# Kernel tuning notes

Measured on AMD Instinct MI355X. Metric: run time of the kernel, lower is better.

Reference implementation:

```python
import jax, jax.numpy as jnp
import numpy as np

B, T, D, H, O = 32768, 96, 7, 3, 7

def setup_inputs() -> dict:
    key = jax.random.key(0)
    ks = jax.random.split(key, 7)
    s_ih = 1.0 / np.sqrt(H)
    inp = {
        "x": jax.random.normal(ks[0], (B, T, D), dtype=jnp.float32),
        # PyTorch nn.LSTM params (gate order i,f,g,o), uniform(-1/sqrt(H), 1/sqrt(H))
        "W_ih": jax.random.uniform(ks[1], (4 * H, D), jnp.float32, -s_ih, s_ih),
        "W_hh": jax.random.uniform(ks[2], (4 * H, H), jnp.float32, -s_ih, s_ih),
        "b_ih": jax.random.uniform(ks[3], (4 * H,), jnp.float32, -s_ih, s_ih),
        "b_hh": jax.random.uniform(ks[4], (4 * H,), jnp.float32, -s_ih, s_ih),
        # nn.Linear(H*T, O*T): weight [out,in]
        "W_lin": jax.random.uniform(ks[5], (O * T, H * T), jnp.float32, -1.0 / np.sqrt(H * T), 1.0 / np.sqrt(H * T)),
        "b_lin": jax.random.uniform(ks[6], (O * T,), jnp.float32, -1.0 / np.sqrt(H * T), 1.0 / np.sqrt(H * T)),
    }
    return inp

def _lstm(x, W_ih, W_hh, b_ih, b_hh):
    b = x.shape[0]
    h0 = jnp.zeros((b, H), x.dtype)
    c0 = jnp.zeros((b, H), x.dtype)
    bias = b_ih + b_hh

    def step(carry, x_t):
        h, c = carry
        gates = x_t @ W_ih.T + h @ W_hh.T + bias  # [b, 4H]
        i, f, g, o = jnp.split(gates, 4, axis=-1)
        i = jax.nn.sigmoid(i)
        f = jax.nn.sigmoid(f)
        g = jnp.tanh(g)
        o = jax.nn.sigmoid(o)
        c = f * c + i * g
        h = o * jnp.tanh(c)
        return (h, c), h

    (_, _), hs = jax.lax.scan(step, (h0, c0), jnp.swapaxes(x, 0, 1))  # hs: [T, b, H]
    return jnp.swapaxes(hs, 0, 1)  # [b, T, H]

def reference(x, W_ih, W_hh, b_ih, b_hh, W_lin, b_lin):
    out = _lstm(x, W_ih, W_hh, b_ih, b_hh)            # [B, T, H]
    out = out.reshape(x.shape[0], -1)                  # [B, T*H]
    out = out @ W_lin.T + b_lin                        # [B, O*T]
    return out.reshape(x.shape)                        # [B, T, D]
```

## Files before the change

kernel.cpp:

```cpp
#include <hip/hip_runtime.h>
#include <stdint.h>

typedef unsigned short u16;
typedef unsigned int u32;
typedef __attribute__((ext_vector_type(8))) __bf16 bf16x8;
typedef __attribute__((ext_vector_type(4))) float f32x4;

#define B_TOT   32768
#define T_SEQ   96
#define D_IN    7
#define K_LIN   288
#define N_LIN   672
#define N_PAD   768

#define LOG2E      1.4426950408889634f
#define TWO_LOG2E  2.8853900817779268f

__device__ __forceinline__ u16 f2bf(float f) {
  u32 u = __builtin_bit_cast(u32, f);
  u += 0x7fffu + ((u >> 16) & 1u);
  return (u16)(u >> 16);
}
template<int Q>
__device__ __forceinline__ float qbcast(float v) {
  int i = __builtin_bit_cast(int, v);
  i = __builtin_amdgcn_update_dpp(0, i, Q * 0x55, 0xF, 0xF, true);
  return __builtin_bit_cast(float, i);
}
template<int CTRL>
__device__ __forceinline__ float rdpp(float v) {
  int i = __builtin_bit_cast(int, v);
  i = __builtin_amdgcn_update_dpp(0, i, CTRL, 0xF, 0xF, true);
  return __builtin_bit_cast(float, i);
}

__global__ __launch_bounds__(256) void convert_kernel(
    const float* __restrict__ Wlin, const float* __restrict__ blin,
    u16* __restrict__ Bw, float* __restrict__ biasp)
{
  int i = blockIdx.x * 256 + threadIdx.x;
  if (i < N_PAD * K_LIN) {
    int n = i / K_LIN;
    int kk = i - n * K_LIN;
    int jm = kk / T_SEQ;
    int tm = kk - jm * T_SEQ;
    Bw[i] = f2bf((n < N_LIN) ? Wlin[n * K_LIN + tm * 3 + jm] : 0.0f);
  }
  if (i < N_PAD) biasp[i] = (i < N_LIN) ? blin[i] : 0.0f;
}

__device__ __forceinline__ void steps8_gp(
    const float* __restrict__ xc,
    float& h, float& c,
    const float (&wih)[7], const float (&whr)[4], float bias,
    float sel_s, float sel_b, float* hv8)
{
#pragma unroll
  for (int s = 0; s < 8; ++s) {
    float z = bias;
#pragma unroll
    for (int k = 0; k < 7; ++k) z = fmaf(xc[s * 7 + k], wih[k], z);
    float r1 = rdpp<0x124>(h);
    float r2 = rdpp<0x128>(h);
    float r3 = rdpp<0x12C>(h);
    z = fmaf(h,  whr[0], z);
    z = fmaf(r1, whr[1], z);
    z = fmaf(r2, whr[2], z);
    z = fmaf(r3, whr[3], z);
    float sg = __builtin_amdgcn_rcpf(1.0f + __builtin_amdgcn_exp2f(z));
    float a = fmaf(sel_s, sg, sel_b);
    float ai = qbcast<0>(a);
    float af = qbcast<1>(a);
    float ag = qbcast<2>(a);
    float ao = qbcast<3>(a);
    c = fmaf(af, c, ai * ag);
    float t = 1.0f - 2.0f * __builtin_amdgcn_rcpf(1.0f + __builtin_amdgcn_exp2f(c * TWO_LOG2E));
    float hv = ao * t;
    hv8[s] = hv;
    h = hv;
  }
}

__global__ __launch_bounds__(256, 8) void lstm_kernel(
    const float* __restrict__ x,
    const float* __restrict__ Wih, const float* __restrict__ Whh,
    const float* __restrict__ bih, const float* __restrict__ bhh,
    u16* __restrict__ hs)
{
  __shared__ float sW[132];
  __shared__ __align__(16) float xb[2][16 * 56];

  const int tid = threadIdx.x;
  for (int i = tid; i < 132; i += 256) {
    float v; int row;
    if (i < 84)       { v = Wih[i];       row = i / 7; }
    else if (i < 120) { v = Whh[i - 84];  row = (i - 84) / 3; }
    else              { v = bih[i - 120] + bhh[i - 120]; row = i - 120; }
    const int G = row / 3;
    sW[i] = v * ((G == 2) ? -TWO_LOG2E : -LOG2E);
  }
  __syncthreads();

  const int sub = tid & 15;
  const int g   = sub & 3;
  const int q   = sub >> 2;
  const int jj  = (q < 3) ? q : 2;
  const int row = g * 3 + jj;

  float wih[7];
#pragma unroll
  for (int k = 0; k < 7; ++k) wih[k] = sW[row * 7 + k];
  float bias = sW[120 + row];

  float pv = (float)q;
  float pr = rdpp<0x124>(pv);
  const int delta = (((int)pr) - q) & 3;

  float whr[4];
  whr[0] = (q < 3) ? sW[84 + row * 3 + q] : 0.0f;
#pragma unroll
  for (int r = 1; r < 4; ++r) {
    const int su = (q + r * delta) & 3;
    whr[r] = (su < 3) ? sW[84 + row * 3 + su] : 0.0f;
  }
  const float sel_s = (g == 2) ? 2.0f : 1.0f;
  const float sel_b = (g == 2) ? -1.0f : 0.0f;
#pragma unroll
  for (int k = 0; k < 7; ++k) asm volatile("" : "+v"(wih[k]));
#pragma unroll
  for (int r = 0; r < 4; ++r) asm volatile("" : "+v"(whr[r]));
  asm volatile("" : "+v"(bias));

  const int b0 = blockIdx.x * 16;
  const bool stager = (tid < 224);
  const int sch = tid / 14;
  const int sof = (tid % 14) * 4;
  const float* gbase = x + (size_t)(b0 + sch) * (T_SEQ * D_IN) + sof;
  float* xw0 = &xb[0][tid * 4];
  float* xw1 = &xb[1][tid * 4];

  const int cc = tid >> 4;
  const float* xc0 = &xb[0][cc * 56];
  const float* xc1 = &xb[1][cc * 56];

  u16* __restrict__ hrow = hs + (size_t)(b0 + cc) * K_LIN + jj * T_SEQ;
  const bool writer = (g == 0) && (q < 3);

  float h = 0.f, c = 0.f;
  float hv8[8];

  if (stager) *(float4*)xw0 = *(const float4*)gbase;
  __syncthreads();

#pragma unroll 1
  for (int n2 = 0; n2 < 6; ++n2) {
    const int n = n2 * 2;
    {
      float4 gpre = {};
      if (stager) gpre = *(const float4*)(gbase + (n + 1) * 56);
      steps8_gp(xc0, h, c, wih, whr, bias, sel_s, sel_b, hv8);
      __builtin_amdgcn_sched_barrier(0);
      if (stager) *(float4*)xw1 = gpre;
      if (writer) {
        u32 w0_, w1_, w2_, w3_;
        asm("v_cvt_pk_bf16_f32 %0, %1, %2" : "=v"(w0_) : "v"(hv8[0]), "v"(hv8[1]));
        asm("v_cvt_pk_bf16_f32 %0, %1, %2" : "=v"(w1_) : "v"(hv8[2]), "v"(hv8[3]));
        asm("v_cvt_pk_bf16_f32 %0, %1, %2" : "=v"(w2_) : "v"(hv8[4]), "v"(hv8[5]));
        asm("v_cvt_pk_bf16_f32 %0, %1, %2" : "=v"(w3_) : "v"(hv8[6]), "v"(hv8[7]));
        uint4 pkv; pkv.x = w0_; pkv.y = w1_; pkv.z = w2_; pkv.w = w3_;
        *(uint4*)(hrow + n * 8) = pkv;
      }
      __syncthreads();
    }
    {
      const bool hn = (n2 < 5);
      float4 gpre = {};
      if (stager && hn) gpre = *(const float4*)(gbase + (n + 2) * 56);
      steps8_gp(xc1, h, c, wih, whr, bias, sel_s, sel_b, hv8);
      __builtin_amdgcn_sched_barrier(0);
      if (stager && hn) *(float4*)xw0 = gpre;
      if (writer) {
        u32 w0_, w1_, w2_, w3_;
        asm("v_cvt_pk_bf16_f32 %0, %1, %2" : "=v"(w0_) : "v"(hv8[0]), "v"(hv8[1]));
        asm("v_cvt_pk_bf16_f32 %0, %1, %2" : "=v"(w1_) : "v"(hv8[2]), "v"(hv8[3]));
        asm("v_cvt_pk_bf16_f32 %0, %1, %2" : "=v"(w2_) : "v"(hv8[4]), "v"(hv8[5]));
        asm("v_cvt_pk_bf16_f32 %0, %1, %2" : "=v"(w3_) : "v"(hv8[6]), "v"(hv8[7]));
        uint4 pkv; pkv.x = w0_; pkv.y = w1_; pkv.z = w2_; pkv.w = w3_;
        *(uint4*)(hrow + (n + 1) * 8) = pkv;
      }
      __syncthreads();
    }
  }
}

__device__ __forceinline__ void gload16(const u16* g, u16* l) {
  __builtin_amdgcn_global_load_lds(
      (const __attribute__((address_space(1))) void*)g,
      (__attribute__((address_space(3))) void*)l, 16, 0, 0);
}

__global__ __launch_bounds__(256) void gemm_kernel(
    const u16* __restrict__ A, const u16* __restrict__ Bw,
    const float* __restrict__ bias, float* __restrict__ C)
{
  __shared__ u16 As[128 * 32];
  __shared__ u16 Bs[128 * 32];
  const int tid  = threadIdx.x;
  const int lane = tid & 63;
  const int wid  = tid >> 6;
  const int wm = wid >> 1, wn = wid & 1;

  int bx = blockIdx.x;
  int swzb = (bx & 7) * 192 + (bx >> 3);
  const int bm = swzb / 6;
  const int bn = swzb - bm * 6;
  const size_t m0 = (size_t)bm * 128;
  const int n0 = bn * 128;

  const int ra = tid >> 2;
  const int ca = (tid & 3) * 8;
  const u16* ga = A  + (m0 + (size_t)ra) * K_LIN + ca;
  const u16* gb = Bw + (size_t)(n0 + ra) * K_LIN + ca;
  u16* lA = &As[wid * 512];
  u16* lB = &Bs[wid * 512];

  const int l15 = lane & 15, l4 = lane >> 4;
  const u16* pAf = &As[(wm * 64 + l15) * 32 + l4 * 8];
  const u16* pBf = &Bs[(wn * 64 + l15) * 32 + l4 * 8];

  f32x4 acc[4][4] = {};

  for (int kt = 0; kt < 9; ++kt) {
    const int ko = kt * 32;
    gload16(ga + ko,               lA);
    gload16(ga + 64 * K_LIN + ko,  lA + 2048);
    gload16(gb + ko,               lB);
    gload16(gb + 64 * K_LIN + ko,  lB + 2048);
    __syncthreads();
    bf16x8 af[4], bfv[4];
#pragma unroll
    for (int i = 0; i < 4; ++i) af[i]  = *(const bf16x8*)(const void*)(pAf + i * 512);
#pragma unroll
    for (int i = 0; i < 4; ++i) bfv[i] = *(const bf16x8*)(const void*)(pBf + i * 512);
#pragma unroll
    for (int mi = 0; mi < 4; ++mi)
#pragma unroll
      for (int ni = 0; ni < 4; ++ni)
        acc[mi][ni] = __builtin_amdgcn_mfma_f32_16x16x32_bf16(af[mi], bfv[ni], acc[mi][ni], 0, 0, 0);
    __syncthreads();
  }

  float bv[4];
#pragma unroll
  for (int ni = 0; ni < 4; ++ni) bv[ni] = bias[n0 + wn * 64 + ni * 16 + l15];

#pragma unroll
  for (int mi = 0; mi < 4; ++mi) {
#pragma unroll
    for (int ni = 0; ni < 4; ++ni) {
      const int col = n0 + wn * 64 + ni * 16 + l15;
      if (col < N_LIN) {
#pragma unroll
        for (int r = 0; r < 4; ++r) {
          const size_t row = m0 + wm * 64 + mi * 16 + l4 * 4 + r;
          C[row * N_LIN + col] = acc[mi][ni][r] + bv[ni];
        }
      }
    }
  }
}

extern "C" void kernel_launch(void* const* d_in, const int* in_sizes, int n_in,
                              void* d_out, int out_size, void* d_ws, size_t ws_size,
                              hipStream_t stream) {
  const float* x    = (const float*)d_in[0];
  const float* Wih  = (const float*)d_in[1];
  const float* Whh  = (const float*)d_in[2];
  const float* bih  = (const float*)d_in[3];
  const float* bhh  = (const float*)d_in[4];
  const float* Wlin = (const float*)d_in[5];
  const float* blin = (const float*)d_in[6];
  float* out = (float*)d_out;

  u16* hs = (u16*)d_ws;
  u16* Bw = (u16*)((char*)d_ws + (size_t)B_TOT * K_LIN * 2);
  float* biasp = (float*)((char*)d_ws + (size_t)B_TOT * K_LIN * 2 + (size_t)N_PAD * K_LIN * 2);

  convert_kernel<<<(N_PAD * K_LIN + 255) / 256, 256, 0, stream>>>(Wlin, blin, Bw, biasp);
  lstm_kernel<<<B_TOT / 16, 256, 0, stream>>>(x, Wih, Whh, bih, bhh, hs);
  gemm_kernel<<<(B_TOT / 128) * (N_PAD / 128), 256, 0, stream>>>(hs, Bw, biasp, out);
}
```

Measured before the change: 82.39 us.

## Process two batch rows per lane with packed f32x2 math in LSTM

```diff
diff --git a/kernel.cpp b/kernel.cpp
--- a/kernel.cpp
+++ b/kernel.cpp
@@ -5,6 +5,7 @@
 typedef unsigned int u32;
 typedef __attribute__((ext_vector_type(8))) __bf16 bf16x8;
 typedef __attribute__((ext_vector_type(4))) float f32x4;
+typedef __attribute__((ext_vector_type(2))) float f32x2;
 
 #define B_TOT   32768
 #define T_SEQ   96
@@ -15,23 +16,25 @@
 
 #define LOG2E      1.4426950408889634f
 #define TWO_LOG2E  2.8853900817779268f
+#define PRSTRIDE   132
 
 __device__ __forceinline__ u16 f2bf(float f) {
   u32 u = __builtin_bit_cast(u32, f);
   u += 0x7fffu + ((u >> 16) & 1u);
   return (u16)(u >> 16);
 }
-template<int Q>
-__device__ __forceinline__ float qbcast(float v) {
-  int i = __builtin_bit_cast(int, v);
-  i = __builtin_amdgcn_update_dpp(0, i, Q * 0x55, 0xF, 0xF, true);
-  return __builtin_bit_cast(float, i);
-}
 template<int CTRL>
-__device__ __forceinline__ float rdpp(float v) {
+__device__ __forceinline__ float rdpp1(float v) {
   int i = __builtin_bit_cast(int, v);
   i = __builtin_amdgcn_update_dpp(0, i, CTRL, 0xF, 0xF, true);
   return __builtin_bit_cast(float, i);
+}
+template<int CTRL>
+__device__ __forceinline__ f32x2 rdpp2(f32x2 v) {
+  f32x2 r;
+  r.x = rdpp1<CTRL>(v.x);
+  r.y = rdpp1<CTRL>(v.y);
+  return r;
 }
 
 __global__ __launch_bounds__(256) void convert_kernel(
@@ -49,46 +52,76 @@
   if (i < N_PAD) biasp[i] = (i < N_LIN) ? blin[i] : 0.0f;
 }
 
-__device__ __forceinline__ void steps8_gp(
+__device__ __forceinline__ void steps8_pk(
     const float* __restrict__ xc,
-    float& h, float& c,
-    const float (&wih)[7], const float (&whr)[4], float bias,
-    float sel_s, float sel_b, float* hv8)
+    f32x2& h, f32x2& c,
+    const f32x2 (&wih)[7], const f32x2 (&whr)[4], f32x2 bias,
+    f32x2 sels, f32x2 selb, f32x2* hv8)
 {
 #pragma unroll
   for (int s = 0; s < 8; ++s) {
-    float z = bias;
-#pragma unroll
-    for (int k = 0; k < 7; ++k) z = fmaf(xc[s * 7 + k], wih[k], z);
-    float r1 = rdpp<0x124>(h);
-    float r2 = rdpp<0x128>(h);
-    float r3 = rdpp<0x12C>(h);
-    z = fmaf(h,  whr[0], z);
-    z = fmaf(r1, whr[1], z);
-    z = fmaf(r2, whr[2], z);
-    z = fmaf(r3, whr[3], z);
-    float sg = __builtin_amdgcn_rcpf(1.0f + __builtin_amdgcn_exp2f(z));
-    float a = fmaf(sel_s, sg, sel_b);
-    float ai = qbcast<0>(a);
-    float af = qbcast<1>(a);
-    float ag = qbcast<2>(a);
-    float ao = qbcast<3>(a);
-    c = fmaf(af, c, ai * ag);
-    float t = 1.0f - 2.0f * __builtin_amdgcn_rcpf(1.0f + __builtin_amdgcn_exp2f(c * TWO_LOG2E));
-    float hv = ao * t;
+    const f32x2* xs = (const f32x2*)(xc + s * 16);
+    f32x2 z = bias;
+#pragma unroll
+    for (int k = 0; k < 7; ++k) z = xs[k] * wih[k] + z;
+    f32x2 r1 = rdpp2<0x124>(h);
+    f32x2 r2 = rdpp2<0x128>(h);
+    f32x2 r3 = rdpp2<0x12C>(h);
+    z = h  * whr[0] + z;
+    z = r1 * whr[1] + z;
+    z = r2 * whr[2] + z;
+    z = r3 * whr[3] + z;
+    f32x2 sg;
+    sg.x = __builtin_amdgcn_rcpf(1.0f + __builtin_amdgcn_exp2f(z.x));
+    sg.y = __builtin_amdgcn_rcpf(1.0f + __builtin_amdgcn_exp2f(z.y));
+    f32x2 a = sels * sg + selb;
+    f32x2 ai = rdpp2<0x00>(a);
+    f32x2 af = rdpp2<0x55>(a);
+    f32x2 ag = rdpp2<0xAA>(a);
+    f32x2 ao = rdpp2<0xFF>(a);
+    c = af * c + ai * ag;
+    f32x2 t;
+    t.x = 1.0f - 2.0f * __builtin_amdgcn_rcpf(1.0f + __builtin_amdgcn_exp2f(c.x * TWO_LOG2E));
+    t.y = 1.0f - 2.0f * __builtin_amdgcn_rcpf(1.0f + __builtin_amdgcn_exp2f(c.y * TWO_LOG2E));
+    f32x2 hv = ao * t;
     hv8[s] = hv;
     h = hv;
   }
 }
 
-__global__ __launch_bounds__(256, 8) void lstm_kernel(
+__device__ __forceinline__ void stw(float* base, const int (&offs)[4],
+                                    float4 a, float4 b) {
+  f32x2 v;
+  v.x = a.x; v.y = b.x; *(f32x2*)(base + offs[0]) = v;
+  v.x = a.y; v.y = b.y; *(f32x2*)(base + offs[1]) = v;
+  v.x = a.z; v.y = b.z; *(f32x2*)(base + offs[2]) = v;
+  v.x = a.w; v.y = b.w; *(f32x2*)(base + offs[3]) = v;
+}
+
+__device__ __forceinline__ void wrchunk(u16* hrA, u16* hrB, int n, const f32x2* hv8) {
+  u32 a0, a1, a2, a3, c0, c1, c2, c3;
+  asm("v_cvt_pk_bf16_f32 %0, %1, %2" : "=v"(a0) : "v"(hv8[0].x), "v"(hv8[1].x));
+  asm("v_cvt_pk_bf16_f32 %0, %1, %2" : "=v"(a1) : "v"(hv8[2].x), "v"(hv8[3].x));
+  asm("v_cvt_pk_bf16_f32 %0, %1, %2" : "=v"(a2) : "v"(hv8[4].x), "v"(hv8[5].x));
+  asm("v_cvt_pk_bf16_f32 %0, %1, %2" : "=v"(a3) : "v"(hv8[6].x), "v"(hv8[7].x));
+  asm("v_cvt_pk_bf16_f32 %0, %1, %2" : "=v"(c0) : "v"(hv8[0].y), "v"(hv8[1].y));
+  asm("v_cvt_pk_bf16_f32 %0, %1, %2" : "=v"(c1) : "v"(hv8[2].y), "v"(hv8[3].y));
+  asm("v_cvt_pk_bf16_f32 %0, %1, %2" : "=v"(c2) : "v"(hv8[4].y), "v"(hv8[5].y));
+  asm("v_cvt_pk_bf16_f32 %0, %1, %2" : "=v"(c3) : "v"(hv8[6].y), "v"(hv8[7].y));
+  uint4 pa; pa.x = a0; pa.y = a1; pa.z = a2; pa.w = a3;
+  uint4 pb; pb.x = c0; pb.y = c1; pb.z = c2; pb.w = c3;
+  *(uint4*)(hrA + n * 8) = pa;
+  *(uint4*)(hrB + n * 8) = pb;
+}
+
+__global__ __launch_bounds__(256, 4) void lstm_kernel(
     const float* __restrict__ x,
     const float* __restrict__ Wih, const float* __restrict__ Whh,
     const float* __restrict__ bih, const float* __restrict__ bhh,
     u16* __restrict__ hs)
 {
   __shared__ float sW[132];
-  __shared__ __align__(16) float xb[2][16 * 56];
+  __shared__ __align__(16) float xb[2][16 * PRSTRIDE];
 
   const int tid = threadIdx.x;
   for (int i = tid; i < 132; i += 256) {
@@ -107,87 +140,91 @@
   const int jj  = (q < 3) ? q : 2;
   const int row = g * 3 + jj;
 
-  float wih[7];
-#pragma unroll
-  for (int k = 0; k < 7; ++k) wih[k] = sW[row * 7 + k];
-  float bias = sW[120 + row];
-
   float pv = (float)q;
-  float pr = rdpp<0x124>(pv);
+  float pr = rdpp1<0x124>(pv);
   const int delta = (((int)pr) - q) & 3;
 
-  float whr[4];
-  whr[0] = (q < 3) ? sW[84 + row * 3 + q] : 0.0f;
-#pragma unroll
-  for (int r = 1; r < 4; ++r) {
-    const int su = (q + r * delta) & 3;
-    whr[r] = (su < 3) ? sW[84 + row * 3 + su] : 0.0f;
-  }
-  const float sel_s = (g == 2) ? 2.0f : 1.0f;
-  const float sel_b = (g == 2) ? -1.0f : 0.0f;
+  f32x2 wih[7], whr[4], bias2;
+#pragma unroll
+  for (int k = 0; k < 7; ++k) { float w = sW[row * 7 + k]; wih[k].x = w; wih[k].y = w; }
+  { float b = sW[120 + row]; bias2.x = b; bias2.y = b; }
+  {
+    float w0 = (q < 3) ? sW[84 + row * 3 + q] : 0.0f;
+    whr[0].x = w0; whr[0].y = w0;
+#pragma unroll
+    for (int r = 1; r < 4; ++r) {
+      const int su = (q + r * delta) & 3;
+      float w = (su < 3) ? sW[84 + row * 3 + su] : 0.0f;
+      whr[r].x = w; whr[r].y = w;
+    }
+  }
+  f32x2 sels, selb;
+  { float ss = (g == 2) ? 2.0f : 1.0f, sb = (g == 2) ? -1.0f : 0.0f;
+    sels.x = ss; sels.y = ss; selb.x = sb; selb.y = sb; }
 #pragma unroll
   for (int k = 0; k < 7; ++k) asm volatile("" : "+v"(wih[k]));
 #pragma unroll
   for (int r = 0; r < 4; ++r) asm volatile("" : "+v"(whr[r]));
-  asm volatile("" : "+v"(bias));
-
-  const int b0 = blockIdx.x * 16;
+  asm volatile("" : "+v"(bias2));
+
+  const int b0c = blockIdx.x * 32;
   const bool stager = (tid < 224);
-  const int sch = tid / 14;
+  const int p   = tid / 14;
   const int sof = (tid % 14) * 4;
-  const float* gbase = x + (size_t)(b0 + sch) * (T_SEQ * D_IN) + sof;
-  float* xw0 = &xb[0][tid * 4];
-  float* xw1 = &xb[1][tid * 4];
-
-  const int cc = tid >> 4;
-  const float* xc0 = &xb[0][cc * 56];
-  const float* xc1 = &xb[1][cc * 56];
-
-  u16* __restrict__ hrow = hs + (size_t)(b0 + cc) * K_LIN + jj * T_SEQ;
+  const float* gA = x + (size_t)(b0c + 2 * p) * (T_SEQ * D_IN) + sof;
+  const float* gB = gA + T_SEQ * D_IN;
+  int offs[4];
+#pragma unroll
+  for (int i = 0; i < 4; ++i) {
+    const int v = sof + i;
+    const int s = (v * 9363) >> 16;
+    const int k = v - s * 7;
+    offs[i] = p * PRSTRIDE + s * 16 + k * 2;
+  }
+
+  const int pp = tid >> 4;
+  const float* xc0 = &xb[0][pp * PRSTRIDE];
+  const float* xc1 = &xb[1][pp * PRSTRIDE];
+  u16* hrA = hs + (size_t)(b0c + 2 * pp) * K_LIN + jj * T_SEQ;
+  u16* hrB = hrA + K_LIN;
   const bool writer = (g == 0) && (q < 3);
 
-  float h = 0.f, c = 0.f;
-  float hv8[8];
-
-  if (stager) *(float4*)xw0 = *(const float4*)gbase;
+  f32x2 h = {0.f, 0.f}, c = {0.f, 0.f};
+  f32x2 hv8[8];
+
+  if (stager) {
+    float4 a = *(const float4*)gA;
+    float4 b = *(const float4*)gB;
+    stw(&xb[0][0], offs, a, b);
+  }
   __syncthreads();
 
 #pragma unroll 1
   for (int n2 = 0; n2 < 6; ++n2) {
     const int n = n2 * 2;
     {
-      float4 gpre = {};
-      if (stager) gpre = *(const float4*)(gbase + (n + 1) * 56);
-      steps8_gp(xc0, h, c, wih, whr, bias, sel_s, sel_b, hv8);
+      float4 pa = {}, pb = {};
+      if (stager) {
+        pa = *(const float4*)(gA + (n + 1) * 56);
+        pb = *(const float4*)(gB + (n + 1) * 56);
+      }
+      steps8_pk(xc0, h, c, wih, whr, bias2, sels, selb, hv8);
       __builtin_amdgcn_sched_barrier(0);
-      if (stager) *(float4*)xw1 = gpre;
-      if (writer) {
-        u32 w0_, w1_, w2_, w3_;
-        asm("v_cvt_pk_bf16_f32 %0, %1, %2" : "=v"(w0_) : "v"(hv8[0]), "v"(hv8[1]));
-        asm("v_cvt_pk_bf16_f32 %0, %1, %2" : "=v"(w1_) : "v"(hv8[2]), "v"(hv8[3]));
-        asm("v_cvt_pk_bf16_f32 %0, %1, %2" : "=v"(w2_) : "v"(hv8[4]), "v"(hv8[5]));
-        asm("v_cvt_pk_bf16_f32 %0, %1, %2" : "=v"(w3_) : "v"(hv8[6]), "v"(hv8[7]));
-        uint4 pkv; pkv.x = w0_; pkv.y = w1_; pkv.z = w2_; pkv.w = w3_;
-        *(uint4*)(hrow + n * 8) = pkv;
-      }
+      if (stager) stw(&xb[1][0], offs, pa, pb);
+      if (writer) wrchunk(hrA, hrB, n, hv8);
       __syncthreads();
     }
     {
       const bool hn = (n2 < 5);
-      float4 gpre = {};
-      if (stager && hn) gpre = *(const float4*)(gbase + (n + 2) * 56);
-      steps8_gp(xc1, h, c, wih, whr, bias, sel_s, sel_b, hv8);
+      float4 pa = {}, pb = {};
+      if (stager && hn) {
+        pa = *(const float4*)(gA + (n + 2) * 56);
+        pb = *(const float4*)(gB + (n + 2) * 56);
+      }
+      steps8_pk(xc1, h, c, wih, whr, bias2, sels, selb, hv8);
       __builtin_amdgcn_sched_barrier(0);
-      if (stager && hn) *(float4*)xw0 = gpre;
-      if (writer) {
-        u32 w0_, w1_, w2_, w3_;
-        asm("v_cvt_pk_bf16_f32 %0, %1, %2" : "=v"(w0_) : "v"(hv8[0]), "v"(hv8[1]));
-        asm("v_cvt_pk_bf16_f32 %0, %1, %2" : "=v"(w1_) : "v"(hv8[2]), "v"(hv8[3]));
-        asm("v_cvt_pk_bf16_f32 %0, %1, %2" : "=v"(w2_) : "v"(hv8[4]), "v"(hv8[5]));
-        asm("v_cvt_pk_bf16_f32 %0, %1, %2" : "=v"(w3_) : "v"(hv8[6]), "v"(hv8[7]));
-        uint4 pkv; pkv.x = w0_; pkv.y = w1_; pkv.z = w2_; pkv.w = w3_;
-        *(uint4*)(hrow + (n + 1) * 8) = pkv;
-      }
+      if (stager && hn) stw(&xb[0][0], offs, pa, pb);
+      if (writer) wrchunk(hrA, hrB, n + 1, hv8);
       __syncthreads();
     }
   }
@@ -262,8 +299,8 @@
       if (col < N_LIN) {
 #pragma unroll
         for (int r = 0; r < 4; ++r) {
-          const size_t row = m0 + wm * 64 + mi * 16 + l4 * 4 + r;
-          C[row * N_LIN + col] = acc[mi][ni][r] + bv[ni];
+          const size_t rowi = m0 + wm * 64 + mi * 16 + l4 * 4 + r;
+          C[rowi * N_LIN + col] = acc[mi][ni][r] + bv[ni];
         }
       }
     }
@@ -287,6 +324,6 @@
   float* biasp = (float*)((char*)d_ws + (size_t)B_TOT * K_LIN * 2 + (size_t)N_PAD * K_LIN * 2);
 
   convert_kernel<<<(N_PAD * K_LIN + 255) / 256, 256, 0, stream>>>(Wlin, blin, Bw, biasp);
-  lstm_kernel<<<B_TOT / 16, 256, 0, stream>>>(x, Wih, Whh, bih, bhh, hs);
+  lstm_kernel<<<B_TOT / 32, 256, 0, stream>>>(x, Wih, Whh, bih, bhh, hs);
   gemm_kernel<<<(B_TOT / 128) * (N_PAD / 128), 256, 0, stream>>>(hs, Bw, biasp, out);
 }
```

Measured after the change: 84.05 us. +2.0%, slower.
